# Performance work log

Measured on AMD Instinct MI355X. Metric: run time of the kernel, lower is better.

## Reference

```python
import jax, jax.numpy as jnp
import numpy as np
import math

B, S, D, H, DFF = 4, 1024, 1024, 16, 4096
DH = D // H
ALPHA = 1.0
NEG = -1e20
EPS = 1e-5


def layernorm(x, g, b):
    mu = jnp.mean(x, axis=-1, keepdims=True)
    var = jnp.mean((x - mu) ** 2, axis=-1, keepdims=True)
    return (x - mu) * jax.lax.rsqrt(var + EPS) * g + b


def setup_inputs() -> dict:
    key = jax.random.key(0)
    ks = jax.random.split(key, 16)
    sc = 1.0 / math.sqrt(D)
    inp = {
        "x": jax.random.normal(ks[0], (B, S, D), jnp.float32),
        "mask": jnp.ones((B, 1, S), jnp.float32),
        "Wq": jax.random.normal(ks[1], (D, D), jnp.float32) * sc,
        "Wk": jax.random.normal(ks[2], (D, D), jnp.float32) * sc,
        "Wv": jax.random.normal(ks[3], (D, D), jnp.float32) * sc,
        "ln1_g": jnp.ones((DH,), jnp.float32),
        "ln1_b": jnp.zeros((DH,), jnp.float32),
        "Wo": jax.random.normal(ks[4], (D, D), jnp.float32) * sc,
        "bo": jnp.zeros((D,), jnp.float32),
        "ln2_g": jnp.ones((D,), jnp.float32),
        "ln2_b": jnp.zeros((D,), jnp.float32),
        "Ws": jax.random.normal(ks[5], (D, D), jnp.float32) * sc,
        "Wh": jax.random.normal(ks[6], (D, D), jnp.float32) * sc,
        "b_f": jnp.zeros((D,), jnp.float32),
        "lnfg_g": jnp.ones((D,), jnp.float32),
        "lnfg_b": jnp.zeros((D,), jnp.float32),
        "Wp1": jax.random.normal(ks[7], (DFF, D), jnp.float32) * sc,
        "bp1": jnp.zeros((DFF,), jnp.float32),
        "Wp2": jax.random.normal(ks[8], (D, DFF), jnp.float32) / math.sqrt(DFF),
        "bp2": jnp.zeros((D,), jnp.float32),
        "lnffn_g": jnp.ones((D,), jnp.float32),
        "lnffn_b": jnp.zeros((D,), jnp.float32),
    }
    return inp


def reference(x, mask, Wq, Wk, Wv, ln1_g, ln1_b, Wo, bo, ln2_g, ln2_b,
              Ws, Wh, b_f, lnfg_g, lnfg_b, Wp1, bp1, Wp2, bp2, lnffn_g, lnffn_b):
    b, s, d = x.shape
    # --- masked multi-head attention ---
    q = (x @ Wq.T).reshape(b, s, H, DH)
    k = (x @ Wk.T).reshape(b, s, H, DH)
    v = (x @ Wv.T).reshape(b, s, H, DH)
    q = layernorm(q, ln1_g, ln1_b)
    k = layernorm(k, ln1_g, ln1_b)
    v = layernorm(v, ln1_g, ln1_b)
    energy = jnp.einsum('nqhd,nkhd->nhqk', q, k)  # (B,H,S,S)
    # directional mask: forward pass -> strictly lower triangular allowed (0), else -1e20
    idx = jnp.arange(s)
    allowed = idx[:, None] > idx[None, :]  # tril(diagonal=-1)
    dir_mask = jnp.where(allowed, 0.0, NEG).astype(x.dtype)  # (S,S)
    m = jnp.broadcast_to(mask, (b, H, s))  # (B,H,S)
    pair = m[:, :, :, None] * m[:, :, None, :]  # (B,H,S,S)
    final_mask = pair * dir_mask[None, None]
    dist_mask = -jnp.abs(idx[:, None] - idx[None, :]).astype(x.dtype)  # (S,S)
    pre = energy / math.sqrt(d) + final_mask + ALPHA * dist_mask[None, None]
    attn = jax.nn.softmax(pre, axis=-1)
    # faithful to source einsum 'nhql,nlhd->nlhd' (sums attention over q)
    out = jnp.einsum('nhql,nlhd->nlhd', attn, v)
    out = out.reshape(b, s, d)
    out = out @ Wo.T + bo
    h = layernorm(out, ln2_g, ln2_b)
    # --- fusion gate and norm ---
    s_f = layernorm(x @ Ws.T, lnfg_g, lnfg_b)
    h_f = layernorm(h @ Wh.T, lnfg_g, lnfg_b)
    f = jax.nn.sigmoid(s_f + h_f + b_f)
    g = layernorm(f * s_f + (1.0 - f) * h_f, lnfg_g, lnfg_b)
    # --- position-wise FFN + residual + norm ---
    ff = jax.nn.relu(g @ Wp1.T + bp1) @ Wp2.T + bp2
    return layernorm(ff + g, lnffn_g, lnffn_b)
```

## Files before the change

### kernel.cpp

```cpp
#include <hip/hip_runtime.h>

constexpr int CB   = 4;
constexpr int CS   = 1024;
constexpr int CD   = 1024;
constexpr int CH   = 16;
constexpr int CDFF = 4096;
constexpr int CNT  = CB * CS;

typedef unsigned short ush;
typedef __bf16 bf16_t;
typedef bf16_t bf16x8 __attribute__((ext_vector_type(8)));
typedef float  f32x4  __attribute__((ext_vector_type(4)));

__device__ __forceinline__ ush f2bf(float f) {
    union { float f; unsigned u; } v; v.f = f;
    unsigned u = v.u;
    return (ush)((u + 0x7fffu + ((u >> 16) & 1u)) >> 16);
}
__device__ __forceinline__ float bf2f(ush h) {
    union { unsigned u; float f; } v; v.u = ((unsigned)h) << 16;
    return v.f;
}
__device__ __forceinline__ void ub8(uint4 v, float* d) {
    d[0] = bf2f((ush)v.x); d[1] = bf2f((ush)(v.x >> 16));
    d[2] = bf2f((ush)v.y); d[3] = bf2f((ush)(v.y >> 16));
    d[4] = bf2f((ush)v.z); d[5] = bf2f((ush)(v.z >> 16));
    d[6] = bf2f((ush)v.w); d[7] = bf2f((ush)(v.w >> 16));
}
__device__ __forceinline__ uint4 pb8(const float* d) {
    uint4 v;
    v.x = (unsigned)f2bf(d[0]) | ((unsigned)f2bf(d[1]) << 16);
    v.y = (unsigned)f2bf(d[2]) | ((unsigned)f2bf(d[3]) << 16);
    v.z = (unsigned)f2bf(d[4]) | ((unsigned)f2bf(d[5]) << 16);
    v.w = (unsigned)f2bf(d[6]) | ((unsigned)f2bf(d[7]) << 16);
    return v;
}

__device__ __forceinline__ void gll16(const void* g, void* l) {
    __builtin_amdgcn_global_load_lds((const __attribute__((address_space(1))) void*)g,
                                     (__attribute__((address_space(3))) void*)l,
                                     16, 0, 0);
}

constexpr int Q4 = (CD * CD) / 4;
__global__ __launch_bounds__(256) void k_convert_all(
        const float4* __restrict__ Wq, const float4* __restrict__ Wk,
        const float4* __restrict__ Wv, const float4* __restrict__ Ws,
        const float4* __restrict__ Wo, const float4* __restrict__ Wh,
        const float4* __restrict__ Wp1, const float4* __restrict__ Wp2,
        const float4* __restrict__ x, uint4* __restrict__ arena,
        uint4* __restrict__ xb, float4* __restrict__ wz) {
    int i = blockIdx.x * 256 + threadIdx.x;
    int stride = gridDim.x * 256;
    for (int i2 = i; i2 < (CB * CH * CS) / 4; i2 += stride)
        wz[i2] = (float4){0.f, 0.f, 0.f, 0.f};
    for (; i < 9 * Q4; i += stride) {
        const int F = i * 2;
        const int seg = F >> 18;
        const float4* src; int off;
        if (seg < 6) {
            src = (seg == 0) ? Wq : (seg == 1) ? Wk : (seg == 2) ? Wv
                : (seg == 3) ? Ws : (seg == 4) ? Wo : Wh;
            off = F & (Q4 - 1);
        } else if (seg < 10) { src = Wp1; off = F - 6 * Q4; }
        else if (seg < 14)   { src = Wp2; off = F - 10 * Q4; }
        else                 { src = x;   off = F - 14 * Q4; }
        float4 a = src[off], b = src[off + 1];
        uint4 o;
        o.x = (unsigned)f2bf(a.x) | ((unsigned)f2bf(a.y) << 16);
        o.y = (unsigned)f2bf(a.z) | ((unsigned)f2bf(a.w) << 16);
        o.z = (unsigned)f2bf(b.x) | ((unsigned)f2bf(b.y) << 16);
        o.w = (unsigned)f2bf(b.z) | ((unsigned)f2bf(b.w) << 16);
        if (seg < 14) arena[i] = o;
        else          xb[i - 7 * Q4] = o;
    }
}

template <int TN, int EPI, int SPLITK>
__global__ __launch_bounds__(256, 4) void k_gemm_bt(
        const ush* __restrict__ A, const ush* __restrict__ Bm,
        ush* __restrict__ Cb,
        const float* __restrict__ bias, const float* __restrict__ bias2,
        ush* __restrict__ out2, ush* __restrict__ out3, ush* __restrict__ sb,
        int N, int K) {
    constexpr int NJ  = TN / 32;
    constexpr int BCH = TN / 32;
    constexpr int EPS = TN + 8;
    constexpr int STG = (128 + TN) * 64;
    constexpr int LDS_USH = (STG > 128 * EPS) ? STG : 128 * EPS;
    __shared__ ush smem[LDS_USH];
    ush* As = smem;
    ush* Bs = smem + 128 * 64;
    ush* Cs = smem;

    const int tid  = threadIdx.x;
    const int wave = tid >> 6, lane = tid & 63;
    const int quad = lane >> 4, r = lane & 15;
    const int wm = wave >> 1, wn = wave & 1;
    const int bm = blockIdx.x, bn = blockIdx.y;

    const int kcnt  = K / SPLITK;
    const int kbase = blockIdx.z * kcnt;
    ush* dst0 = Cb;
    if (SPLITK > 1) dst0 += (size_t)blockIdx.z * (size_t)gridDim.x * 128 * N;

    const int trow = tid >> 3, tk8 = tid & 7;
    const int kcl  = tk8 ^ (trow & 7);
    const ush* ap = A  + (size_t)(bm * 128 + trow) * K + kbase + kcl * 8;
    const ush* bp = Bm + (size_t)(bn * TN  + trow) * K + kbase + kcl * 8;
    ush* asd = As + tid * 8;
    ush* bsd = Bs + tid * 8;
    const size_t cstep = (size_t)32 * K;

    f32x4 acc[4][NJ];
#pragma unroll
    for (int i = 0; i < 4; i++)
#pragma unroll
        for (int j = 0; j < NJ; j++) acc[i][j] = (f32x4){0.f, 0.f, 0.f, 0.f};

    const int rx = r & 7;
    for (int k0 = 0; k0 < kcnt; k0 += 64) {
#pragma unroll
        for (int c = 0; c < 4; c++)   gll16(ap + c * cstep, asd + c * 2048);
#pragma unroll
        for (int c = 0; c < BCH; c++) gll16(bp + c * cstep, bsd + c * 2048);
        ap += 64; bp += 64;
        __syncthreads();
#pragma unroll
        for (int h = 0; h < 2; h++) {
            const int kx = (((h << 2) | quad) ^ rx) * 8;
            bf16x8 af[4], bfv[NJ];
#pragma unroll
            for (int i = 0; i < 4; i++)
                af[i] = *(const bf16x8*)(As + (wm * 64 + i * 16 + r) * 64 + kx);
#pragma unroll
            for (int j = 0; j < NJ; j++)
                bfv[j] = *(const bf16x8*)(Bs + (wn * (TN / 2) + j * 16 + r) * 64 + kx);
#pragma unroll
            for (int i = 0; i < 4; i++)
#pragma unroll
                for (int j = 0; j < NJ; j++)
                    acc[i][j] = __builtin_amdgcn_mfma_f32_16x16x32_bf16(af[i], bfv[j], acc[i][j], 0, 0, 0);
        }
        __syncthreads();
    }

    if (EPI == 4 && bn < 24) {
        float g4[4], b4[4];
#pragma unroll
        for (int j = 0; j < 4; j++) { g4[j] = bias[j * 16 + r]; b4[j] = bias2[j * 16 + r]; }
#pragma unroll
        for (int i = 0; i < 4; i++) {
            const int row = wm * 64 + i * 16 + quad * 4;
#pragma unroll
            for (int g = 0; g < 4; g++) {
                float s = 0.f, q = 0.f;
#pragma unroll
                for (int j = 0; j < 4; j++) { float v = acc[i][j][g]; s += v; q += v * v; }
                s += __shfl_xor(s, 1); q += __shfl_xor(q, 1);
                s += __shfl_xor(s, 2); q += __shfl_xor(q, 2);
                s += __shfl_xor(s, 4); q += __shfl_xor(q, 4);
                s += __shfl_xor(s, 8); q += __shfl_xor(q, 8);
                float mu   = s * (1.f / 64.f);
                float rstd = rsqrtf(q * (1.f / 64.f) - mu * mu + 1e-5f);
#pragma unroll
                for (int j = 0; j < 4; j++) {
                    float y = (acc[i][j][g] - mu) * rstd * g4[j] + b4[j];
                    Cs[(row + g) * EPS + wn * 64 + j * 16 + r] = f2bf(y);
                }
            }
        }
    } else {
#pragma unroll
        for (int i = 0; i < 4; i++) {
            const int row = wm * 64 + i * 16 + quad * 4;
#pragma unroll
            for (int j = 0; j < NJ; j++) {
                const int col = wn * (TN / 2) + j * 16 + r;
                float bv = (EPI == 3) ? bias[bn * TN + col] : 0.f;
#pragma unroll
                for (int g = 0; g < 4; g++) {
                    float v = acc[i][j][g] + bv;
                    if (EPI == 3) v = fmaxf(v, 0.f);
                    Cs[(row + g) * EPS + col] = f2bf(v);
                }
            }
        }
    }
    __syncthreads();

    ush* dst = dst0;
    int colbase = bn * TN, Nn = N;
    if (EPI == 4) {
        Nn = 1024;
        if (bn < 8)       { dst = Cb;   colbase = bn * 128; }
        else if (bn < 16) { dst = out2; colbase = (bn - 8) * 128; }
        else if (bn < 24) { dst = out3; colbase = (bn - 16) * 128; }
        else              { dst = sb;   colbase = (bn - 24) * 128; }
    }
    const int tpr = TN / 8;
    const int rpp = 2048 / TN;
    const int srow2 = tid / tpr;
    const int scol2 = (tid % tpr) * 8;
#pragma unroll
    for (int pp = 0; pp < TN / 16; pp++) {
        const int rr = pp * rpp + srow2;
        uint4 vv = *(const uint4*)&Cs[rr * EPS + scol2];
        *(uint4*)&dst[(size_t)(bm * 128 + rr) * Nn + colbase + scol2] = vv;
    }
}

__global__ __launch_bounds__(256) void k_attn(const ush* __restrict__ qb,
                                              const ush* __restrict__ kb,
                                              const float* __restrict__ mask,
                                              float* __restrict__ wcol) {
    __shared__ ush   Qs[64][72];
    __shared__ ush   Ks[64][72];
    __shared__ float colpart[4][64];

    const int tid  = threadIdx.x;
    const int wave = tid >> 6, lane = tid & 63;
    const int quad = lane >> 4, r = lane & 15;
    const int bh = blockIdx.x, bi = bh >> 4, hi = bh & 15;
    const int q0 = blockIdx.y * 64;

    {
        int row = tid >> 2, seg = (tid & 3) * 16;
        const ush* src = qb + ((size_t)(bi * CS + q0 + row) * CD + hi * 64 + seg);
        *(uint4*)&Qs[row][seg]     = *(const uint4*)src;
        *(uint4*)&Qs[row][seg + 8] = *(const uint4*)(src + 8);
    }
    __syncthreads();
    bf16x8 af0 = *(const bf16x8*)&Qs[wave * 16 + r][quad * 8];
    bf16x8 af1 = *(const bf16x8*)&Qs[wave * 16 + r][32 + quad * 8];

    float mq[4];
#pragma unroll
    for (int g = 0; g < 4; g++) mq[g] = mask[bi * CS + q0 + wave * 16 + quad * 4 + g];

    float pr[2][4][4];
    float s_loc[4] = {0.f, 0.f, 0.f, 0.f};

#pragma unroll
    for (int t = 0; t < 2; t++) {
        const int l0 = q0 - 64 + t * 64;
        if (l0 >= 0) {
            __syncthreads();
            {
                int row = tid >> 2, seg = (tid & 3) * 16;
                const ush* src = kb + ((size_t)(bi * CS + l0 + row) * CD + hi * 64 + seg);
                *(uint4*)&Ks[row][seg]     = *(const uint4*)src;
                *(uint4*)&Ks[row][seg + 8] = *(const uint4*)(src + 8);
            }
            __syncthreads();
#pragma unroll
            for (int jt = 0; jt < 4; jt++) {
                bf16x8 bf0 = *(const bf16x8*)&Ks[jt * 16 + r][quad * 8];
                bf16x8 bf1 = *(const bf16x8*)&Ks[jt * 16 + r][32 + quad * 8];
                f32x4 sc = (f32x4){0.f, 0.f, 0.f, 0.f};
                sc = __builtin_amdgcn_mfma_f32_16x16x32_bf16(af0, bf0, sc, 0, 0, 0);
                sc = __builtin_amdgcn_mfma_f32_16x16x32_bf16(af1, bf1, sc, 0, 0, 0);
                const int l = l0 + jt * 16 + r;
                const float ml = mask[bi * CS + l];
#pragma unroll
                for (int g = 0; g < 4; g++) {
                    const int qg = q0 + wave * 16 + quad * 4 + g;
                    float e  = sc[g] * 0.03125f;
                    float mv = (qg > l) ? 0.f : mq[g] * ml * (-1e20f);
                    float p  = __expf(e + mv - fabsf((float)(qg - l)) - 8.f);
                    pr[t][jt][g] = p;
                    s_loc[g] += p;
                }
            }
        }
    }

    float rs[4];
#pragma unroll
    for (int g = 0; g < 4; g++) {
        float s = s_loc[g];
        s += __shfl_xor(s, 1); s += __shfl_xor(s, 2);
        s += __shfl_xor(s, 4); s += __shfl_xor(s, 8);
        rs[g] = (s > 0.f) ? 1.f / s : 0.f;
    }

#pragma unroll
    for (int t = 0; t < 2; t++) {
        const int l0 = q0 - 64 + t * 64;
        if (l0 >= 0) {
#pragma unroll
            for (int jt = 0; jt < 4; jt++) {
                float csum = 0.f;
#pragma unroll
                for (int g = 0; g < 4; g++) csum += pr[t][jt][g] * rs[g];
                csum += __shfl_xor(csum, 16);
                csum += __shfl_xor(csum, 32);
                if (quad == 0) colpart[wave][jt * 16 + r] = csum;
            }
            __syncthreads();
            if (tid < 64) {
                float v = colpart[0][tid] + colpart[1][tid] + colpart[2][tid] + colpart[3][tid];
                atomicAdd(&wcol[(size_t)bh * CS + l0 + tid], v);
            }
            __syncthreads();
        }
    }
}

__global__ __launch_bounds__(256) void k_scale_v(const ush* __restrict__ vb,
                                                 const float* __restrict__ wcol,
                                                 ush* __restrict__ out) {
    const int g = blockIdx.x * 256 + threadIdx.x;
    const int token = g >> 7;
    const int cg = g & 127;
    const int c0 = cg * 8, h = cg >> 3;
    const int l = token & (CS - 1), b = token >> 10;
    const float w = wcol[(size_t)(b * CH + h) * CS + l] + (1.f / 1024.f);
    float d[8];
    ub8(*(const uint4*)&vb[(size_t)token * CD + c0], d);
#pragma unroll
    for (int j = 0; j < 8; j++) d[j] *= w;
    *(uint4*)&out[(size_t)token * CD + c0] = pb8(d);
}

__device__ __forceinline__ void stats128(float s, float q, float* red,
                                         int wave, int lane, float& mu, float& rstd) {
#pragma unroll
    for (int off = 32; off >= 1; off >>= 1) {
        s += __shfl_xor(s, off);
        q += __shfl_xor(q, off);
    }
    if (lane == 0) { red[wave] = s; red[2 + wave] = q; }
    __syncthreads();
    s = red[0] + red[1];
    q = red[2] + red[3];
    mu = s * (1.f / 1024.f);
    rstd = rsqrtf(q * (1.f / 1024.f) - mu * mu + 1e-5f);
    __syncthreads();
}

template <int MODE>
__global__ __launch_bounds__(128) void k_ln_row(const ush* __restrict__ b0,
                                                const ush* __restrict__ b1,
                                                const ush* __restrict__ b2,
                                                const float* __restrict__ badd,
                                                const float* __restrict__ gam,
                                                const float* __restrict__ bet,
                                                float* __restrict__ outf,
                                                ush* __restrict__ outb) {
    __shared__ float red[4];
    const int tid = threadIdx.x, wave = tid >> 6, lane = tid & 63;
    const size_t base = (size_t)blockIdx.x * CD;
    const int c0 = tid * 8;
    float t[8], sr[8], tmp[8], gv[8], bv[8];
    float s = 0.f, q = 0.f, mu, rstd;

    *(float4*)&gv[0] = *(const float4*)&gam[c0];
    *(float4*)&gv[4] = *(const float4*)&gam[c0 + 4];
    *(float4*)&bv[0] = *(const float4*)&bet[c0];
    *(float4*)&bv[4] = *(const float4*)&bet[c0 + 4];

    if (MODE == 2) {
        float av[8];
        *(float4*)&av[0] = *(const float4*)&badd[c0];
        *(float4*)&av[4] = *(const float4*)&badd[c0 + 4];
        ub8(*(const uint4*)&b0[base + c0], sr);
        ub8(*(const uint4*)&b1[base + c0], t);
        ub8(*(const uint4*)&b2[base + c0], tmp);
#pragma unroll
        for (int j = 0; j < 8; j++) t[j] += tmp[j];
#pragma unroll
        for (int j = 0; j < 8; j++) { s += sr[j]; q += sr[j] * sr[j]; }
        stats128(s, q, red, wave, lane, mu, rstd);
#pragma unroll
        for (int j = 0; j < 8; j++) sr[j] = (sr[j] - mu) * rstd * gv[j] + bv[j];
        s = 0.f; q = 0.f;
#pragma unroll
        for (int j = 0; j < 8; j++) { s += t[j]; q += t[j] * t[j]; }
        stats128(s, q, red, wave, lane, mu, rstd);
#pragma unroll
        for (int j = 0; j < 8; j++) {
            float hf = (t[j] - mu) * rstd * gv[j] + bv[j];
            float f  = 1.f / (1.f + __expf(-(sr[j] + hf + av[j])));
            t[j] = f * sr[j] + (1.f - f) * hf;
        }
    } else {
        float av[8];
        *(float4*)&av[0] = *(const float4*)&badd[c0];
        *(float4*)&av[4] = *(const float4*)&badd[c0 + 4];
        ub8(*(const uint4*)&b0[base + c0], t);
        ub8(*(const uint4*)&b1[base + c0], tmp);
#pragma unroll
        for (int j = 0; j < 8; j++) t[j] += tmp[j] + av[j];
        if (MODE == 3) {
            ub8(*(const uint4*)&b2[base + c0], tmp);
#pragma unroll
            for (int j = 0; j < 8; j++) t[j] += tmp[j];
        }
    }

    s = 0.f; q = 0.f;
#pragma unroll
    for (int j = 0; j < 8; j++) { s += t[j]; q += t[j] * t[j]; }
    stats128(s, q, red, wave, lane, mu, rstd);

    float y[8];
#pragma unroll
    for (int j = 0; j < 8; j++) y[j] = (t[j] - mu) * rstd * gv[j] + bv[j];
    if (MODE == 3) {
        *(float4*)&outf[base + c0]     = *(float4*)&y[0];
        *(float4*)&outf[base + c0 + 4] = *(float4*)&y[4];
    } else {
        *(uint4*)&outb[base + c0] = pb8(y);
    }
}

extern "C" void kernel_launch(void* const* d_in, const int* in_sizes, int n_in,
                              void* d_out, int out_size, void* d_ws, size_t ws_size,
                              hipStream_t stream) {
    const float* x    = (const float*)d_in[0];
    const float* mask = (const float*)d_in[1];
    const float* Wq   = (const float*)d_in[2];
    const float* Wk   = (const float*)d_in[3];
    const float* Wv   = (const float*)d_in[4];
    const float* ln1g = (const float*)d_in[5];
    const float* ln1b = (const float*)d_in[6];
    const float* Wo   = (const float*)d_in[7];
    const float* bo   = (const float*)d_in[8];
    const float* ln2g = (const float*)d_in[9];
    const float* ln2b = (const float*)d_in[10];
    const float* Ws   = (const float*)d_in[11];
    const float* Wh   = (const float*)d_in[12];
    const float* bf_  = (const float*)d_in[13];
    const float* lnfgg = (const float*)d_in[14];
    const float* lnfgb = (const float*)d_in[15];
    const float* Wp1  = (const float*)d_in[16];
    const float* bp1  = (const float*)d_in[17];
    const float* Wp2  = (const float*)d_in[18];
    const float* bp2  = (const float*)d_in[19];
    const float* lnffg = (const float*)d_in[20];
    const float* lnffb = (const float*)d_in[21];
    float* out = (float*)d_out;

    char* p = (char*)d_ws;
    auto alloc = [&](size_t bytes) -> char* {
        char* r = p;
        p += (bytes + 255) & ~(size_t)255;
        return r;
    };
    ush*   arena = (ush*)alloc((size_t)14 * CD * CD * 2);
    ush*   Wob   = arena + (size_t)4 * CD * CD;
    ush*   Whb   = arena + (size_t)5 * CD * CD;
    ush*   Wp1b  = arena + (size_t)6 * CD * CD;
    ush*   Wp2b  = arena + (size_t)10 * CD * CD;
    ush*   xb    = (ush*)alloc((size_t)CNT * CD * 2);
    ush*   klnb  = (ush*)alloc((size_t)CNT * CD * 2);
    ush*   vb    = (ush*)alloc((size_t)CNT * CD * 2);
    ush*   qlnb  = (ush*)alloc((size_t)CNT * CD * 2);
    ush*   gb    = (ush*)alloc((size_t)CNT * CD * 2);
    ush*   P     = (ush*)alloc((size_t)2 * CNT * CD * 2);
    ush*   P1    = P + (size_t)CNT * CD;
    ush*   ff1b  = (ush*)alloc((size_t)CNT * CDFF * 2);
    float* wcol  = (float*)alloc((size_t)CB * CH * CS * 4);
    ush*   sbuf  = ff1b;
    ush*   attb  = qlnb;
    ush*   hb    = klnb;

    dim3 blk(256);

    k_convert_all<<<dim3(4608), blk, 0, stream>>>(
        (const float4*)Wq, (const float4*)Wk, (const float4*)Wv, (const float4*)Ws,
        (const float4*)Wo, (const float4*)Wh, (const float4*)Wp1, (const float4*)Wp2,
        (const float4*)x, (uint4*)arena, (uint4*)xb, (float4*)wcol);

    k_gemm_bt<128, 4, 1><<<dim3(32, 32, 1), blk, 0, stream>>>(
        xb, arena, qlnb, ln1g, ln1b, klnb, vb, sbuf, 4096, CD);

    k_attn<<<dim3(CB * CH, CS / 64), blk, 0, stream>>>(qlnb, klnb, mask, wcol);
    k_scale_v<<<dim3(CNT * CD / 8 / 256), blk, 0, stream>>>(vb, wcol, attb);

    k_gemm_bt<64, 0, 2><<<dim3(32, 16, 2), blk, 0, stream>>>(
        attb, Wob, P, nullptr, nullptr, nullptr, nullptr, nullptr, CD, CD);
    k_ln_row<0><<<dim3(CNT), dim3(128), 0, stream>>>(P, P1, nullptr, bo, ln2g, ln2b, nullptr, hb);

    k_gemm_bt<64, 0, 2><<<dim3(32, 16, 2), blk, 0, stream>>>(
        hb, Whb, P, nullptr, nullptr, nullptr, nullptr, nullptr, CD, CD);
    k_ln_row<2><<<dim3(CNT), dim3(128), 0, stream>>>(sbuf, P, P1, bf_, lnfgg, lnfgb, nullptr, gb);

    k_gemm_bt<128, 3, 1><<<dim3(32, 32, 1), blk, 0, stream>>>(
        gb, Wp1b, ff1b, bp1, nullptr, nullptr, nullptr, nullptr, CDFF, CD);
    k_gemm_bt<64, 0, 2><<<dim3(32, 16, 2), blk, 0, stream>>>(
        ff1b, Wp2b, P, nullptr, nullptr, nullptr, nullptr, nullptr, CD, CDFF);
    k_ln_row<3><<<dim3(CNT), dim3(128), 0, stream>>>(P, P1, gb, bp2, lnffg, lnffb, out, nullptr);

    (void)in_sizes; (void)n_in; (void)out_size; (void)ws_size;
}
```

Measured before the change: 338.9 us.

## Fuse V column-weight scaling into attention kernel via per-chunk completion counters

Removes the separate k_scale_v launch and does the V scaling inside k_attn. Each attention block bumps atomic ready counters for its own 64-row key chunk and the chunk before it. Whichever block arrives last for a chunk scales that chunk's V rows by the finished column weights and writes them to attb. This saves a kernel launch and the extra pass over wcol and V, in exchange for atomics, a threadfence and a tail of extra work in some blocks. The counters are zeroed in the existing conversion kernel by extending its zero-fill range.

```diff
diff --git a/kernel.cpp b/kernel.cpp
--- a/kernel.cpp
+++ b/kernel.cpp
@@ -43,6 +43,7 @@
 }
 
 constexpr int Q4 = (CD * CD) / 4;
+constexpr int WZ4 = (CB * CH * CS) / 4 + 256;
 __global__ __launch_bounds__(256) void k_convert_all(
         const float4* __restrict__ Wq, const float4* __restrict__ Wk,
         const float4* __restrict__ Wv, const float4* __restrict__ Ws,
@@ -52,7 +53,7 @@
         uint4* __restrict__ xb, float4* __restrict__ wz) {
     int i = blockIdx.x * 256 + threadIdx.x;
     int stride = gridDim.x * 256;
-    for (int i2 = i; i2 < (CB * CH * CS) / 4; i2 += stride)
+    for (int i2 = i; i2 < WZ4; i2 += stride)
         wz[i2] = (float4){0.f, 0.f, 0.f, 0.f};
     for (; i < 9 * Q4; i += stride) {
         const int F = i * 2;
@@ -213,10 +214,14 @@
 __global__ __launch_bounds__(256) void k_attn(const ush* __restrict__ qb,
                                               const ush* __restrict__ kb,
                                               const float* __restrict__ mask,
-                                              float* __restrict__ wcol) {
+                                              float* __restrict__ wcol,
+                                              int* __restrict__ ready,
+                                              const ush* __restrict__ vb,
+                                              ush* __restrict__ attb) {
     __shared__ ush   Qs[64][72];
     __shared__ ush   Ks[64][72];
     __shared__ float colpart[4][64];
+    __shared__ int   winner[2];
 
     const int tid  = threadIdx.x;
     const int wave = tid >> 6, lane = tid & 63;
@@ -230,6 +235,7 @@
         *(uint4*)&Qs[row][seg]     = *(const uint4*)src;
         *(uint4*)&Qs[row][seg + 8] = *(const uint4*)(src + 8);
     }
+    if (tid < 2) winner[tid] = 0;
     __syncthreads();
     bf16x8 af0 = *(const bf16x8*)&Qs[wave * 16 + r][quad * 8];
     bf16x8 af1 = *(const bf16x8*)&Qs[wave * 16 + r][32 + quad * 8];
@@ -305,22 +311,42 @@
             __syncthreads();
         }
     }
-}
-
-__global__ __launch_bounds__(256) void k_scale_v(const ush* __restrict__ vb,
-                                                 const float* __restrict__ wcol,
-                                                 ush* __restrict__ out) {
-    const int g = blockIdx.x * 256 + threadIdx.x;
-    const int token = g >> 7;
-    const int cg = g & 127;
-    const int c0 = cg * 8, h = cg >> 3;
-    const int l = token & (CS - 1), b = token >> 10;
-    const float w = wcol[(size_t)(b * CH + h) * CS + l] + (1.f / 1024.f);
-    float d[8];
-    ub8(*(const uint4*)&vb[(size_t)token * CD + c0], d);
-#pragma unroll
-    for (int j = 0; j < 8; j++) d[j] *= w;
-    *(uint4*)&out[(size_t)token * CD + c0] = pb8(d);
+
+    __threadfence();
+    const int yc = q0 >> 6;
+    if (tid == 0) {
+        int old = __hip_atomic_fetch_add(&ready[bh * 16 + yc], 1,
+                                         __ATOMIC_ACQ_REL, __HIP_MEMORY_SCOPE_AGENT);
+        const int need = (yc == 15) ? 1 : 2;
+        if (old == need - 1) winner[1] = 1;
+    } else if (tid == 64 && yc >= 1) {
+        int old = __hip_atomic_fetch_add(&ready[bh * 16 + yc - 1], 1,
+                                         __ATOMIC_ACQ_REL, __HIP_MEMORY_SCOPE_AGENT);
+        if (old == 1) winner[0] = 1;
+    }
+    __syncthreads();
+#pragma unroll
+    for (int wsel = 0; wsel < 2; wsel++) {
+        if (winner[wsel]) {
+            const int c  = yc - 1 + wsel;
+            const int lr = c * 64 + (tid >> 2);
+            const int cc = hi * 64 + (tid & 3) * 16;
+            const float w = __hip_atomic_load(&wcol[(size_t)bh * CS + lr],
+                                              __ATOMIC_RELAXED, __HIP_MEMORY_SCOPE_AGENT)
+                          + (1.f / 1024.f);
+            const ush* vsrc = vb   + (size_t)(bi * CS + lr) * CD + cc;
+            ush*       vdst = attb + (size_t)(bi * CS + lr) * CD + cc;
+            float d[8];
+            ub8(*(const uint4*)vsrc, d);
+#pragma unroll
+            for (int j = 0; j < 8; j++) d[j] *= w;
+            *(uint4*)vdst = pb8(d);
+            ub8(*(const uint4*)(vsrc + 8), d);
+#pragma unroll
+            for (int j = 0; j < 8; j++) d[j] *= w;
+            *(uint4*)(vdst + 8) = pb8(d);
+        }
+    }
 }
 
 __device__ __forceinline__ void stats128(float s, float q, float* red,
@@ -461,7 +487,8 @@
     ush*   P     = (ush*)alloc((size_t)2 * CNT * CD * 2);
     ush*   P1    = P + (size_t)CNT * CD;
     ush*   ff1b  = (ush*)alloc((size_t)CNT * CDFF * 2);
-    float* wcol  = (float*)alloc((size_t)CB * CH * CS * 4);
+    float* wcol  = (float*)alloc((size_t)CB * CH * CS * 4 + 1024 * 4);
+    int*   ready = (int*)(wcol + (size_t)CB * CH * CS);
     ush*   sbuf  = ff1b;
     ush*   attb  = qlnb;
     ush*   hb    = klnb;
@@ -476,8 +503,8 @@
     k_gemm_bt<128, 4, 1><<<dim3(32, 32, 1), blk, 0, stream>>>(
         xb, arena, qlnb, ln1g, ln1b, klnb, vb, sbuf, 4096, CD);
 
-    k_attn<<<dim3(CB * CH, CS / 64), blk, 0, stream>>>(qlnb, klnb, mask, wcol);
-    k_scale_v<<<dim3(CNT * CD / 8 / 256), blk, 0, stream>>>(vb, wcol, attb);
+    k_attn<<<dim3(CB * CH, CS / 64), blk, 0, stream>>>(
+        qlnb, klnb, mask, wcol, ready, vb, attb);
 
     k_gemm_bt<64, 0, 2><<<dim3(32, 16, 2), blk, 0, stream>>>(
         attb, Wob, P, nullptr, nullptr, nullptr, nullptr, nullptr, CD, CD);
```

New measurement: 466.4 us. 37.6% more time.
